# Performance work log

Measured on AMD Instinct MI355X. Metric: run time of the kernel, lower is better.

## Reference

```python
import jax, jax.numpy as jnp
import numpy as np

CLIP = 5.0  # clip_value from init


def setup_inputs() -> dict:
    key = jax.random.key(0)
    ks = jax.random.split(key, 6)
    B, T, I, H = 128, 1024, 256, 512
    s = 1.0 / np.sqrt(H)
    return {
        "x": jax.random.normal(ks[0], (B, T, I), dtype=jnp.float32),
        "h0": jax.random.normal(ks[1], (1, H), dtype=jnp.float32),
        "w_ih": jax.random.normal(ks[2], (3 * H, I), dtype=jnp.float32) * s,
        "w_hh": jax.random.normal(ks[3], (3 * H, H), dtype=jnp.float32) * s,
        "b_ih": jax.random.normal(ks[4], (3 * H,), dtype=jnp.float32) * s,
        "b_hh": jax.random.normal(ks[5], (3 * H,), dtype=jnp.float32) * s,
    }


def reference(x, h0, w_ih, w_hh, b_ih, b_hh):
    # x: [B, T, I], h0: [1, H]
    B = x.shape[0]
    h_init = jnp.tile(h0, (B, 1))  # [B, H]
    # Precompute all input projections in one big GEMM: [T, B, 3H]
    gi_all = jnp.einsum('bti,gi->tbg', x, w_ih) + b_ih

    def step(h, gi):
        gh = h @ w_hh.T + b_hh                      # [B, 3H]
        ir, iz, inn = jnp.split(gi, 3, axis=-1)
        hr, hz, hn = jnp.split(gh, 3, axis=-1)
        r = jax.nn.sigmoid(ir + hr)
        z = jax.nn.sigmoid(iz + hz)
        n = jnp.tanh(inn + r * hn)
        h_new = (1.0 - z) * n + z * h
        h_new = jnp.clip(h_new, -CLIP, CLIP)
        return h_new, h_new

    h_last, out = jax.lax.scan(step, h_init, gi_all)  # out: [T, B, H]
    output = jnp.transpose(out, (1, 0, 2))            # [B, T, H]
    return output, h_last
```

## Files before the change

kernel.cpp:

```cpp
#include <hip/hip_runtime.h>
#include <math.h>

#define T_SEQ 1024
#define B_SZ  128
#define I_SZ  256
#define H_SZ  512
#define G_SZ  1536

#define NBS   8
#define MB    16
#define NHS   8
#define HB    64
#define GB    192
#define NTHR  384
#define PGB   384
#define PH    (MB * H_SZ)
#define SLC   (3 * PH)

#define SENT32 0x7FFF7FFFu

typedef _Float16 f16;
typedef _Float16 half8 __attribute__((ext_vector_type(8)));
typedef _Float16 f16x4 __attribute__((ext_vector_type(4)));
typedef float f32x4 __attribute__((ext_vector_type(4)));
typedef unsigned uint32x2 __attribute__((ext_vector_type(2)));
typedef unsigned uint32x4 __attribute__((ext_vector_type(4)));

__device__ __forceinline__ f32x4 cload_f4(const void* p) {
    f32x4 v;
    asm volatile("global_load_dwordx4 %0, %1, off sc0 sc1" : "=v"(v) : "v"(p));
    return v;
}
__device__ __forceinline__ void cstore_f4(void* p, f32x4 v) {
    asm volatile("global_store_dwordx4 %0, %1, off sc0 sc1" :: "v"(p), "v"(v) : "memory");
}
__device__ __forceinline__ void cstore_u2(void* p, uint32x2 v) {
    asm volatile("global_store_dwordx2 %0, %1, off sc0 sc1" :: "v"(p), "v"(v) : "memory");
}
__device__ __forceinline__ f16x4 load_f16x4_nw(const void* p) {
    f16x4 v;
    asm volatile("global_load_dwordx2 %0, %1, off" : "=v"(v) : "v"(p));
    return v;
}
__device__ __forceinline__ void wait_vm0() {
    asm volatile("s_waitcnt vmcnt(0)" ::: "memory");
    __builtin_amdgcn_sched_barrier(0);
}
__device__ __forceinline__ bool stale4(f32x4 v) {
    uint32x4 u = __builtin_bit_cast(uint32x4, v);
    return (u[0] == SENT32) | (u[1] == SENT32) | (u[2] == SENT32) | (u[3] == SENT32);
}

__global__ void setup_kernel(const float* __restrict__ w_ih,
                             const float* __restrict__ w_hh,
                             const float* __restrict__ h0,
                             f16* __restrict__ wp16,
                             f16* __restrict__ wf16,
                             f16* __restrict__ hbuf) {
    const int i0 = blockIdx.x * blockDim.x + threadIdx.x;
    const int stride = gridDim.x * blockDim.x;
    for (int i = i0; i < I_SZ * G_SZ; i += stride)
        wp16[i] = (f16)w_ih[i];
    for (int i = i0; i < NHS * GB * H_SZ; i += stride) {
        int hs  = i / (GB * H_SZ);
        int rem = i % (GB * H_SZ);
        int gl = rem / H_SZ, k = rem % H_SZ;
        int gate = gl >> 6, c = gl & 63;
        int gg = gate * H_SZ + hs * HB + c;
        wf16[i] = (f16)w_hh[(size_t)gg * H_SZ + k];
    }
    const int htot = NBS * SLC;
    const f16 sent = __builtin_bit_cast(f16, (unsigned short)0x7FFF);
    for (int i = i0; i < htot; i += stride) {
        int j = i % SLC;
        int phase = j / PH;
        hbuf[i] = (phase == 0) ? (f16)h0[j & (H_SZ - 1)] : sent;
    }
}

__global__ __launch_bounds__(512, 1)
void proj_kernel(const float* __restrict__ x,
                 const f16* __restrict__ wp16,
                 const float* __restrict__ b_ih,
                 f16* __restrict__ gi16) {
    const int t  = blockIdx.x >> 2;
    const int g0 = (blockIdx.x & 3) * PGB;
    const int tid  = threadIdx.x;
    const int wid  = tid >> 6;
    const int lane = tid & 63;
    const int col  = lane & 15;
    const int krow = lane >> 4;

    __shared__ __align__(16) unsigned char x_lds[128 * 512];

    #pragma unroll
    for (int j = 0; j < 8; ++j) {
        int idx = tid + j * 512;
        int b = idx >> 5, k16 = idx & 31;
        const float* xp = x + ((size_t)b * T_SEQ + t) * I_SZ + k16 * 8;
        float4 v0 = *reinterpret_cast<const float4*>(xp);
        float4 v1 = *reinterpret_cast<const float4*>(xp + 4);
        half8 hv;
        hv[0] = (f16)v0.x; hv[1] = (f16)v0.y; hv[2] = (f16)v0.z; hv[3] = (f16)v0.w;
        hv[4] = (f16)v1.x; hv[5] = (f16)v1.y; hv[6] = (f16)v1.z; hv[7] = (f16)v1.w;
        unsigned addr = ((unsigned)(b * 512 + k16 * 16)) ^ (((unsigned)(b & 7)) << 4);
        *reinterpret_cast<half8*>(x_lds + addr) = hv;
    }

    const int gw0 = g0 + wid * 48;
    half8 af[3][8];
    #pragma unroll
    for (int m = 0; m < 3; ++m)
        #pragma unroll
        for (int k = 0; k < 8; ++k)
            af[m][k] = *reinterpret_cast<const half8*>(
                wp16 + (size_t)(gw0 + m * 16 + col) * I_SZ + k * 32 + krow * 8);

    float bias[3][4];
    #pragma unroll
    for (int m = 0; m < 3; ++m)
        #pragma unroll
        for (int r = 0; r < 4; ++r)
            bias[m][r] = b_ih[gw0 + m * 16 + krow * 4 + r];

    __syncthreads();

    #pragma unroll
    for (int nt = 0; nt < 8; ++nt) {
        const int b0 = nt * 16;
        f32x4 acc0 = {0.f,0.f,0.f,0.f}, acc1 = {0.f,0.f,0.f,0.f}, acc2 = {0.f,0.f,0.f,0.f};
        const int brow = b0 + col;
        const unsigned bswz = ((unsigned)(brow & 7)) << 4;
        #pragma unroll
        for (int k = 0; k < 8; ++k) {
            half8 bf = *reinterpret_cast<const half8*>(
                x_lds + (((unsigned)(brow * 512 + k * 64 + krow * 16)) ^ bswz));
            acc0 = __builtin_amdgcn_mfma_f32_16x16x32_f16(af[0][k], bf, acc0, 0, 0, 0);
            acc1 = __builtin_amdgcn_mfma_f32_16x16x32_f16(af[1][k], bf, acc1, 0, 0, 0);
            acc2 = __builtin_amdgcn_mfma_f32_16x16x32_f16(af[2][k], bf, acc2, 0, 0, 0);
        }
        const int pbs = brow >> 4;
        const int pm  = brow & 15;
        #pragma unroll
        for (int r = 0; r < 4; ++r) {
            int gr = gw0 + krow * 4 + r;
            gi16[((size_t)(t * NBS + pbs) * G_SZ + gr)      * MB + pm] = (f16)(acc0[r] + bias[0][r]);
            gi16[((size_t)(t * NBS + pbs) * G_SZ + gr + 16) * MB + pm] = (f16)(acc1[r] + bias[1][r]);
            gi16[((size_t)(t * NBS + pbs) * G_SZ + gr + 32) * MB + pm] = (f16)(acc2[r] + bias[2][r]);
        }
    }
}

__global__ __launch_bounds__(NTHR, 1)
void gru_persist(const f16* __restrict__ gi,
                 const f16* __restrict__ wf16,
                 const float* __restrict__ h0,
                 const float* __restrict__ b_hh,
                 f16* __restrict__ hbuf,
                 float* __restrict__ out) {
    const int bs  = blockIdx.x & (NBS - 1);
    const int hs  = blockIdx.x >> 3;
    const int tid = threadIdx.x;

    __shared__ __align__(16) unsigned char w_lds[96 * 1024];
    __shared__ __align__(16) unsigned char h_lds[MB * H_SZ * 2];
    __shared__ float act_r[MB][HB + 1];
    __shared__ float act_z[MB][HB + 1];
    __shared__ float act_n[MB][HB + 1];
    __shared__ float act_i[MB][HB + 1];

    const int wid  = tid >> 6;
    const int lane = tid & 63;
    const int col  = lane & 15;
    const int krow = lane >> 4;

    const int ttR = wid, ttL = wid + 6;
    const int gateR = ttR >> 2, gateL = ttL >> 2;
    const int gcR = (ttR & 3) * 16 + col;
    const int gcL = (ttL & 3) * 16 + col;
    const int ggR = gateR * H_SZ + hs * HB + gcR;
    const int ggL = gateL * H_SZ + hs * HB + gcL;
    const float biasR = b_hh[ggR];
    const float biasL = b_hh[ggL];

    const f16* wbase = wf16 + (size_t)hs * GB * H_SZ;

    for (int i = tid; i < 96 * 64; i += NTHR) {
        int r = i >> 6, k8 = i & 63;
        f32x4 v = *reinterpret_cast<const f32x4*>(
            wbase + (size_t)(96 + r) * H_SZ + k8 * 8);
        unsigned addr = ((unsigned)(r * 1024 + k8 * 16)) ^ (((unsigned)(r & 7)) << 4);
        *reinterpret_cast<f32x4*>(w_lds + addr) = v;
    }
    half8 bfrag[16];
    {
        const f16* wp = wbase + (size_t)(ttR * 16 + col) * H_SZ + krow * 8;
        #pragma unroll
        for (int kk = 0; kk < 16; ++kk)
            bfrag[kk] = *reinterpret_cast<const half8*>(wp + kk * 32);
    }

    const int cb  = tid >> 4;
    const int cc4 = (tid & 15) * 4;
    f32x4 hm = {0.f, 0.f, 0.f, 0.f};
    if (tid < 256) {
        #pragma unroll
        for (int u = 0; u < 4; ++u) hm[u] = h0[hs * HB + cc4 + u];
    }

    const unsigned a_base = (unsigned)(col * 1024 + krow * 16);
    const unsigned a_swz  = ((unsigned)(col & 7)) << 4;
    const unsigned b_base = (unsigned)((wid * 16 + col) * 1024 + krow * 16);

    const int i0 = tid, i1 = tid + NTHR, i2 = tid + 2 * NTHR;
    const bool has2 = (tid < 256);
    const f32x4 sentv = __builtin_bit_cast(f32x4,
        (uint32x4){SENT32, SENT32, SENT32, SENT32});

    f16* hb = hbuf + (size_t)bs * SLC;

    __syncthreads();

    for (int t = 0; t < T_SEQ; ++t) {
        const size_t pcO = (size_t)(t % 3) * PH;
        const size_t pnO = (size_t)((t + 1) % 3) * PH;
        const size_t paO = (size_t)((t + 2) % 3) * PH;

        f16x4 gvR = load_f16x4_nw(
            gi + ((size_t)(t * NBS + bs) * G_SZ + ggR) * MB + krow * 4);
        f16x4 gvL = load_f16x4_nw(
            gi + ((size_t)(t * NBS + bs) * G_SZ + ggL) * MB + krow * 4);

        const f16* hin = hb + pcO;
        const f16* a0p = hin + (i0 >> 6) * H_SZ + (i0 & 63) * 8;
        const f16* a1p = hin + (i1 >> 6) * H_SZ + (i1 & 63) * 8;
        const f16* a2p = hin + (i2 >> 6) * H_SZ + (i2 & 63) * 8;
        f32x4 v0 = cload_f4(a0p);
        f32x4 v1 = cload_f4(a1p);
        f32x4 v2;
        if (has2) v2 = cload_f4(a2p);
        wait_vm0();
        {
            int guard = 0;
            bool s0 = stale4(v0), s1 = stale4(v1), s2 = has2 && stale4(v2);
            while (__any(s0 | s1 | s2)) {
                if (s0) v0 = cload_f4((const void*)a0p);
                if (s1) v1 = cload_f4((const void*)a1p);
                if (s2) v2 = cload_f4((const void*)a2p);
                wait_vm0();
                s0 = stale4(v0); s1 = stale4(v1); s2 = has2 && stale4(v2);
                if (++guard > (1 << 20)) break;
            }
        }

        {
            unsigned l0 = ((unsigned)((i0 >> 6) * 1024 + (i0 & 63) * 16))
                          ^ (((unsigned)((i0 >> 6) & 7)) << 4);
            *reinterpret_cast<f32x4*>(h_lds + l0) = v0;
            unsigned l1 = ((unsigned)((i1 >> 6) * 1024 + (i1 & 63) * 16))
                          ^ (((unsigned)((i1 >> 6) & 7)) << 4);
            *reinterpret_cast<f32x4*>(h_lds + l1) = v1;
            if (has2) {
                unsigned l2 = ((unsigned)((i2 >> 6) * 1024 + (i2 & 63) * 16))
                              ^ (((unsigned)((i2 >> 6) & 7)) << 4);
                *reinterpret_cast<f32x4*>(h_lds + l2) = v2;
            }
            if (tid < 128) {
                int row = tid >> 3, g = tid & 7;
                cstore_f4(hb + paO + (size_t)row * H_SZ + hs * HB + g * 8, sentv);
            }
        }
        __syncthreads();

        f32x4 accR = {0.f,0.f,0.f,0.f}, accL = {0.f,0.f,0.f,0.f};
        #pragma unroll
        for (int kk = 0; kk < 16; ++kk) {
            half8 av = *reinterpret_cast<const half8*>(
                h_lds + ((a_base + kk * 64) ^ a_swz));
            half8 bv = *reinterpret_cast<const half8*>(
                w_lds + ((b_base + kk * 64) ^ a_swz));
            accR = __builtin_amdgcn_mfma_f32_16x16x32_f16(av, bfrag[kk], accR, 0, 0, 0);
            accL = __builtin_amdgcn_mfma_f32_16x16x32_f16(av, bv,        accL, 0, 0, 0);
        }
        wait_vm0();

        if (gateR == 0) {
            #pragma unroll
            for (int r = 0; r < 4; ++r)
                act_r[krow * 4 + r][gcR] = accR[r] + biasR + (float)gvR[r];
        } else {
            #pragma unroll
            for (int r = 0; r < 4; ++r)
                act_z[krow * 4 + r][gcR] = accR[r] + biasR + (float)gvR[r];
        }
        if (gateL == 1) {
            #pragma unroll
            for (int r = 0; r < 4; ++r)
                act_z[krow * 4 + r][gcL] = accL[r] + biasL + (float)gvL[r];
        } else {
            #pragma unroll
            for (int r = 0; r < 4; ++r) {
                act_n[krow * 4 + r][gcL] = accL[r] + biasL;
                act_i[krow * 4 + r][gcL] = (float)gvL[r];
            }
        }
        __syncthreads();

        if (tid < 256) {
            float h4[4];
            unsigned short us[4];
            #pragma unroll
            for (int u = 0; u < 4; ++u) {
                int c = cc4 + u;
                float r = 1.f / (1.f + __expf(-act_r[cb][c]));
                float z = 1.f / (1.f + __expf(-act_z[cb][c]));
                float a = act_i[cb][c] + r * act_n[cb][c];
                float n = 1.f - 2.f / (__expf(2.f * a) + 1.f);
                float hn = (1.f - z) * n + z * hm[u];
                hn = fminf(fmaxf(hn, -5.f), 5.f);
                hm[u] = hn;
                h4[u] = hn;
                us[u] = __builtin_bit_cast(unsigned short, (f16)hn);
            }
            uint32x2 pk;
            pk[0] = (unsigned)us[0] | ((unsigned)us[1] << 16);
            pk[1] = (unsigned)us[2] | ((unsigned)us[3] << 16);
            const int hg = hs * HB + cc4;
            cstore_u2(hb + pnO + (size_t)cb * H_SZ + hg, pk);

            const int bg = bs * MB + cb;
            *reinterpret_cast<float4*>(
                out + ((size_t)bg * T_SEQ + t) * H_SZ + hg) =
                make_float4(h4[0], h4[1], h4[2], h4[3]);
            if (t == T_SEQ - 1)
                *reinterpret_cast<float4*>(
                    out + (size_t)B_SZ * T_SEQ * H_SZ + (size_t)bg * H_SZ + hg) =
                    make_float4(h4[0], h4[1], h4[2], h4[3]);
        }
    }
}

extern "C" void kernel_launch(void* const* d_in, const int* in_sizes, int n_in,
                              void* d_out, int out_size, void* d_ws, size_t ws_size,
                              hipStream_t stream) {
    const float* x    = (const float*)d_in[0];
    const float* h0   = (const float*)d_in[1];
    const float* w_ih = (const float*)d_in[2];
    const float* w_hh = (const float*)d_in[3];
    const float* b_ih = (const float*)d_in[4];
    const float* b_hh = (const float*)d_in[5];
    float* out = (float*)d_out;

    char* p = (char*)d_ws;
    f16* wp16 = (f16*)p;   p += (size_t)I_SZ * G_SZ * 2;
    f16* wf16 = (f16*)p;   p += (size_t)NHS * GB * H_SZ * 2;
    f16* hbuf = (f16*)p;   p += (size_t)NBS * SLC * 2;
    f16* gi   = (f16*)p;

    setup_kernel<<<512, 256, 0, stream>>>(w_ih, w_hh, h0, wp16, wf16, hbuf);

    proj_kernel<<<T_SEQ * 4, 512, 0, stream>>>(x, wp16, b_ih, gi);

    gru_persist<<<NBS * NHS, NTHR, 0, stream>>>(gi, wf16, h0, b_hh, hbuf, out);
}
```

Before: 3.186 ms.

## Replace triple-buffered hidden-state exchange with per-timestep buffers pre-filled with sentinels

The hidden-state exchange buffer becomes one slot per timestep, (T+1)*NBS*PH halfs, instead of a three-phase ring. The setup kernel now pre-fills every future slot with the sentinel, so the recurrent loop no longer writes a sentinel store each step to re-arm the ring. An s_sleep is added before the polling loads to ease contention on the flag reads. In exchange, setup writes a large buffer of about 128 MB, grows the workspace and launches a larger setup grid, and the sleep adds fixed latency on every step of the serial chain.

```diff
diff --git a/kernel.cpp b/kernel.cpp
--- a/kernel.cpp
+++ b/kernel.cpp
@@ -15,7 +15,6 @@
 #define NTHR  384
 #define PGB   384
 #define PH    (MB * H_SZ)
-#define SLC   (3 * PH)
 
 #define SENT32 0x7FFF7FFFu
 
@@ -31,9 +30,6 @@
     asm volatile("global_load_dwordx4 %0, %1, off sc0 sc1" : "=v"(v) : "v"(p));
     return v;
 }
-__device__ __forceinline__ void cstore_f4(void* p, f32x4 v) {
-    asm volatile("global_store_dwordx4 %0, %1, off sc0 sc1" :: "v"(p), "v"(v) : "memory");
-}
 __device__ __forceinline__ void cstore_u2(void* p, uint32x2 v) {
     asm volatile("global_store_dwordx2 %0, %1, off sc0 sc1" :: "v"(p), "v"(v) : "memory");
 }
@@ -57,25 +53,25 @@
                              f16* __restrict__ wp16,
                              f16* __restrict__ wf16,
                              f16* __restrict__ hbuf) {
-    const int i0 = blockIdx.x * blockDim.x + threadIdx.x;
-    const int stride = gridDim.x * blockDim.x;
-    for (int i = i0; i < I_SZ * G_SZ; i += stride)
+    const size_t i0 = (size_t)blockIdx.x * blockDim.x + threadIdx.x;
+    const size_t stride = (size_t)gridDim.x * blockDim.x;
+    for (size_t i = i0; i < (size_t)I_SZ * G_SZ; i += stride)
         wp16[i] = (f16)w_ih[i];
-    for (int i = i0; i < NHS * GB * H_SZ; i += stride) {
-        int hs  = i / (GB * H_SZ);
-        int rem = i % (GB * H_SZ);
+    for (size_t i = i0; i < (size_t)NHS * GB * H_SZ; i += stride) {
+        int hs  = (int)(i / (GB * H_SZ));
+        int rem = (int)(i % (GB * H_SZ));
         int gl = rem / H_SZ, k = rem % H_SZ;
         int gate = gl >> 6, c = gl & 63;
         int gg = gate * H_SZ + hs * HB + c;
         wf16[i] = (f16)w_hh[(size_t)gg * H_SZ + k];
     }
-    const int htot = NBS * SLC;
-    const f16 sent = __builtin_bit_cast(f16, (unsigned short)0x7FFF);
-    for (int i = i0; i < htot; i += stride) {
-        int j = i % SLC;
-        int phase = j / PH;
-        hbuf[i] = (phase == 0) ? (f16)h0[j & (H_SZ - 1)] : sent;
-    }
+    for (size_t i = i0; i < (size_t)NBS * PH; i += stride)
+        hbuf[i] = (f16)h0[i & (H_SZ - 1)];
+    const uint32x4 sv = {SENT32, SENT32, SENT32, SENT32};
+    const size_t base = (size_t)NBS * PH;
+    const size_t nv   = (size_t)T_SEQ * NBS * PH / 8;
+    for (size_t i = i0; i < nv; i += stride)
+        *reinterpret_cast<uint32x4*>(hbuf + base + i * 8) = sv;
 }
 
 __global__ __launch_bounds__(512, 1)
@@ -214,24 +210,20 @@
 
     const int i0 = tid, i1 = tid + NTHR, i2 = tid + 2 * NTHR;
     const bool has2 = (tid < 256);
-    const f32x4 sentv = __builtin_bit_cast(f32x4,
-        (uint32x4){SENT32, SENT32, SENT32, SENT32});
-
-    f16* hb = hbuf + (size_t)bs * SLC;
 
     __syncthreads();
 
     for (int t = 0; t < T_SEQ; ++t) {
-        const size_t pcO = (size_t)(t % 3) * PH;
-        const size_t pnO = (size_t)((t + 1) % 3) * PH;
-        const size_t paO = (size_t)((t + 2) % 3) * PH;
+        const f16* hin  = hbuf + ((size_t)t       * NBS + bs) * PH;
+        f16*       hpub = hbuf + ((size_t)(t + 1) * NBS + bs) * PH;
 
         f16x4 gvR = load_f16x4_nw(
             gi + ((size_t)(t * NBS + bs) * G_SZ + ggR) * MB + krow * 4);
         f16x4 gvL = load_f16x4_nw(
             gi + ((size_t)(t * NBS + bs) * G_SZ + ggL) * MB + krow * 4);
 
-        const f16* hin = hb + pcO;
+        __builtin_amdgcn_s_sleep(8);
+
         const f16* a0p = hin + (i0 >> 6) * H_SZ + (i0 & 63) * 8;
         const f16* a1p = hin + (i1 >> 6) * H_SZ + (i1 & 63) * 8;
         const f16* a2p = hin + (i2 >> 6) * H_SZ + (i2 & 63) * 8;
@@ -265,10 +257,6 @@
                               ^ (((unsigned)((i2 >> 6) & 7)) << 4);
                 *reinterpret_cast<f32x4*>(h_lds + l2) = v2;
             }
-            if (tid < 128) {
-                int row = tid >> 3, g = tid & 7;
-                cstore_f4(hb + paO + (size_t)row * H_SZ + hs * HB + g * 8, sentv);
-            }
         }
         __syncthreads();
 
@@ -326,7 +314,7 @@
             pk[0] = (unsigned)us[0] | ((unsigned)us[1] << 16);
             pk[1] = (unsigned)us[2] | ((unsigned)us[3] << 16);
             const int hg = hs * HB + cc4;
-            cstore_u2(hb + pnO + (size_t)cb * H_SZ + hg, pk);
+            cstore_u2(hpub + (size_t)cb * H_SZ + hg, pk);
 
             const int bg = bs * MB + cb;
             *reinterpret_cast<float4*>(
@@ -354,10 +342,10 @@
     char* p = (char*)d_ws;
     f16* wp16 = (f16*)p;   p += (size_t)I_SZ * G_SZ * 2;
     f16* wf16 = (f16*)p;   p += (size_t)NHS * GB * H_SZ * 2;
-    f16* hbuf = (f16*)p;   p += (size_t)NBS * SLC * 2;
+    f16* hbuf = (f16*)p;   p += (size_t)(T_SEQ + 1) * NBS * PH * 2;
     f16* gi   = (f16*)p;
 
-    setup_kernel<<<512, 256, 0, stream>>>(w_ih, w_hh, h0, wp16, wf16, hbuf);
+    setup_kernel<<<2048, 256, 0, stream>>>(w_ih, w_hh, h0, wp16, wf16, hbuf);
 
     proj_kernel<<<T_SEQ * 4, 512, 0, stream>>>(x, wp16, b_ih, gi);
 
```

Measured after the change: 2.998 ms. 5.9% less time.
